# Kernel tuning notes

Hardware: AMD Instinct MI355X
Metric: run time of the kernel (lower is better)

The kernel has to match this reference:

```python
import jax, jax.numpy as jnp
import numpy as np

D_MODEL = 512
N_HEADS = 8
HEAD_DIM = D_MODEL // N_HEADS
SEQ = 2048
BATCH = 2
EPS = 1e-5
SCALE = 1.0 / np.sqrt(HEAD_DIM).astype(np.float32)
# (kind, window, dilation) per head, matching init_kwargs head_specs
SPECS = [("global", 0, 1), ("global", 0, 1),
         ("window", 64, 1), ("window", 128, 1), ("window", 256, 1),
         ("dilated", 64, 2), ("dilated", 64, 4), ("dilated", 64, 8)]


def build_masks(N):
    i = jnp.arange(N)
    D = jnp.abs(i[:, None] - i[None, :])
    ms = []
    for kind, w, dil in SPECS:
        if kind == "global":
            ms.append(jnp.ones((N, N), dtype=bool))
        elif kind == "window":
            ms.append(D <= w)
        else:  # dilated
            ms.append((D % dil == 0) & (D // dil <= w))
    return jnp.stack(ms)  # [H, N, N] bool


def layernorm(x, g, b):
    mu = jnp.mean(x, axis=-1, keepdims=True)
    var = jnp.mean((x - mu) ** 2, axis=-1, keepdims=True)
    return (x - mu) * jax.lax.rsqrt(var + EPS) * g + b


def setup_inputs() -> dict:
    key = jax.random.key(0)
    ks = jax.random.split(key, 7)
    w = 0.02
    return {
        "x": jax.random.normal(ks[0], (BATCH, SEQ, D_MODEL), dtype=jnp.float32),
        "Wq": jax.random.normal(ks[1], (D_MODEL, D_MODEL), dtype=jnp.float32) * w,
        "Wk": jax.random.normal(ks[2], (D_MODEL, D_MODEL), dtype=jnp.float32) * w,
        "Wv": jax.random.normal(ks[3], (D_MODEL, D_MODEL), dtype=jnp.float32) * w,
        "Wo": jax.random.normal(ks[4], (D_MODEL, D_MODEL), dtype=jnp.float32) * w,
        "T_w1": jax.random.normal(ks[5], (D_MODEL, D_MODEL), dtype=jnp.float32) * w,
        "T_b1": jnp.zeros((D_MODEL,), dtype=jnp.float32),
        "T_w2": jax.random.normal(ks[6], (1, D_MODEL), dtype=jnp.float32) * w,
        "T_b2": jnp.zeros((1,), dtype=jnp.float32),
        "ln_in_g": jnp.ones((D_MODEL,), dtype=jnp.float32),
        "ln_in_b": jnp.zeros((D_MODEL,), dtype=jnp.float32),
        "ln_out_g": jnp.ones((D_MODEL,), dtype=jnp.float32),
        "ln_out_b": jnp.zeros((D_MODEL,), dtype=jnp.float32),
    }


def reference(x, Wq, Wk, Wv, Wo, T_w1, T_b1, T_w2, T_b2,
              ln_in_g, ln_in_b, ln_out_g, ln_out_b):
    B, N, H = x.shape
    x0 = x
    xn = layernorm(x, ln_in_g, ln_in_b)
    # torch Linear: y = x @ W.T ; reshape to [B, h, N, d]
    def heads(W):
        return (xn @ W.T).reshape(B, N, N_HEADS, HEAD_DIM).transpose(0, 2, 1, 3)
    Q, K, V = heads(Wq), heads(Wk), heads(Wv)
    attn = jnp.einsum("bhqd,bhkd->bhqk", Q, K) * SCALE
    mask = build_masks(N)  # [h, N, N]
    attn = jnp.where(mask[None], attn, -jnp.inf)
    attn = jax.nn.softmax(attn, axis=-1)  # every row has diagonal unmasked
    out = jnp.einsum("bhqk,bhkd->bhqd", attn, V)
    out = out.transpose(0, 2, 1, 3).reshape(B, N, N_HEADS * HEAD_DIM)
    out = out @ Wo.T
    # tanh-gated softmax over sequence dim
    T_logits = jnp.tanh(xn @ T_w1.T + T_b1) @ T_w2.T + T_b2  # [B, N, 1]
    T = jax.nn.softmax(T_logits, axis=1)
    out = out * T
    return layernorm(out + x0, ln_out_g, ln_out_b)
```

## Files before the change

### kernel.cpp

```cpp
#include <hip/hip_runtime.h>
#include <math.h>

#define N_SEQ 2048
#define DM    512
#define NTOK  4096
#define NH    8
#define HD    64
#define NSLOT 18

typedef __attribute__((ext_vector_type(8))) short short8;
typedef __attribute__((ext_vector_type(4))) short short4_t;
typedef __attribute__((ext_vector_type(4))) float f32x4;

__device__ inline short f2bf(float x) {
    union { float f; unsigned u; } v; v.f = x;
    unsigned r = v.u + 0x7fff + ((v.u >> 16) & 1);
    return (short)(r >> 16);
}
__device__ inline float bf2f(short s) {
    union { unsigned u; float f; } v; v.u = ((unsigned)(unsigned short)s) << 16;
    return v.f;
}
__device__ inline unsigned pkbf(float a, float b) {
    return ((unsigned)(unsigned short)f2bf(b) << 16) | (unsigned)(unsigned short)f2bf(a);
}
__device__ inline float ftanh(float x) {
    float e = __expf(2.f * x);
    return 1.f - 2.f / (e + 1.f);
}

__device__ inline f32x4 mfma16(short8 a, short8 b, f32x4 c) {
    return __builtin_amdgcn_mfma_f32_16x16x32_bf16(a, b, c, 0, 0, 0);
}

__device__ __forceinline__ void async_cp16(const short* g, short* l) {
    __builtin_amdgcn_global_load_lds(
        (const __attribute__((address_space(1))) void*)g,
        (__attribute__((address_space(3))) void*)l, 16, 0, 0);
}

__global__ __launch_bounds__(256) void k_lncvt(
    const float* __restrict__ x, const float* __restrict__ g,
    const float* __restrict__ b, short* __restrict__ y, float* __restrict__ lg,
    const float* __restrict__ Wq, const float* __restrict__ Wk,
    const float* __restrict__ Wv, const float* __restrict__ Tw1,
    const float* __restrict__ Wo,
    short* __restrict__ wcat, short* __restrict__ wo) {
    int blk = blockIdx.x, t = threadIdx.x;
    if (blk < 2048) {
        int sub = t >> 7, tt = t & 127;
        int tk = blk * 2 + sub;
        if (tt == 0) lg[tk] = 0.f;
        float4 xv = ((const float4*)(x + (size_t)tk * DM))[tt];
        float s = xv.x + xv.y + xv.z + xv.w;
        float q = xv.x*xv.x + xv.y*xv.y + xv.z*xv.z + xv.w*xv.w;
        for (int o = 32; o; o >>= 1) { s += __shfl_down(s, o); q += __shfl_down(q, o); }
        __shared__ float ls[4], lq[4];
        if ((t & 63) == 0) { ls[t >> 6] = s; lq[t >> 6] = q; }
        __syncthreads();
        s = ls[sub * 2] + ls[sub * 2 + 1];
        q = lq[sub * 2] + lq[sub * 2 + 1];
        float mu = s * (1.f / DM);
        float var = q * (1.f / DM) - mu * mu;
        float rs = rsqrtf(var + 1e-5f);
        float4 gv = ((const float4*)g)[tt], bv = ((const float4*)b)[tt];
        short4_t o;
        o[0] = f2bf((xv.x - mu) * rs * gv.x + bv.x);
        o[1] = f2bf((xv.y - mu) * rs * gv.y + bv.y);
        o[2] = f2bf((xv.z - mu) * rs * gv.z + bv.z);
        o[3] = f2bf((xv.w - mu) * rs * gv.w + bv.w);
        *(short4_t*)&y[(size_t)tk * DM + tt * 4] = o;
    } else {
        int id = (blk - 2048) * 256 + t;
        if (id < 262144) {
            int z = id >> 16; int off = id & 65535;
            const float* s = (z == 0) ? Wq : (z == 1) ? Wk : (z == 2) ? Wv : Tw1;
            float4 v = ((const float4*)s)[off];
            short4_t o = {f2bf(v.x), f2bf(v.y), f2bf(v.z), f2bf(v.w)};
            *(short4_t*)(wcat + (size_t)z * 262144 + (size_t)off * 4) = o;
        } else {
            int off = id - 262144;
            float4 v = ((const float4*)Wo)[off];
            short4_t o = {f2bf(v.x), f2bf(v.y), f2bf(v.z), f2bf(v.w)};
            *(short4_t*)(wo + (size_t)off * 4) = o;
        }
    }
}

__global__ __launch_bounds__(256) void k_gemmqkvt(
    const short* __restrict__ A, const short* __restrict__ W,
    const float* __restrict__ Tb1, const float* __restrict__ Tw2,
    short* __restrict__ qb, short* __restrict__ kb, short* __restrict__ vb,
    float* __restrict__ lg) {
    __shared__ short As[128 * 32];
    __shared__ short Bs[128 * 32];
    int t = threadIdx.x;
    int lane = t & 63, w = t >> 6;
    int wy = w >> 1, wx = w & 1;
    int ln = lane & 15, q4 = lane >> 4;
    int c0 = blockIdx.x * 128, m0 = blockIdx.y * 128;
    int sr = t >> 2, sc = (t & 3) << 3;
    f32x4 acc[4][4];
    f32x4 zero = {0.f, 0.f, 0.f, 0.f};
    #pragma unroll
    for (int i = 0; i < 4; i++)
        #pragma unroll
        for (int j = 0; j < 4; j++) acc[i][j] = zero;
    for (int k0 = 0; k0 < DM; k0 += 32) {
        __syncthreads();
        async_cp16(&A[(size_t)(m0 + sr) * DM + k0 + sc],      &As[sr * 32 + sc]);
        async_cp16(&A[(size_t)(m0 + 64 + sr) * DM + k0 + sc], &As[(64 + sr) * 32 + sc]);
        async_cp16(&W[(size_t)(c0 + sr) * DM + k0 + sc],      &Bs[sr * 32 + sc]);
        async_cp16(&W[(size_t)(c0 + 64 + sr) * DM + k0 + sc], &Bs[(64 + sr) * 32 + sc]);
        __syncthreads();
        short8 af[4], bfr[4];
        #pragma unroll
        for (int i = 0; i < 4; i++)
            af[i] = *(short8*)&As[(wy * 64 + i * 16 + ln) * 32 + q4 * 8];
        #pragma unroll
        for (int j = 0; j < 4; j++)
            bfr[j] = *(short8*)&Bs[(wx * 64 + j * 16 + ln) * 32 + q4 * 8];
        #pragma unroll
        for (int i = 0; i < 4; i++)
            #pragma unroll
            for (int j = 0; j < 4; j++)
                acc[i][j] = mfma16(af[i], bfr[j], acc[i][j]);
    }
    int z = c0 >> 9;
    if (z < 3) {
        short* dst = (z == 0) ? qb : (z == 1) ? kb : vb;
        float sc2 = (z == 0) ? 0.125f : 1.0f;
        #pragma unroll
        for (int i = 0; i < 4; i++)
            #pragma unroll
            for (int j = 0; j < 4; j++)
                #pragma unroll
                for (int r = 0; r < 4; r++) {
                    int row = m0 + wy * 64 + i * 16 + q4 * 4 + r;
                    int col = c0 + wx * 64 + j * 16 + ln;
                    int nin = col & 511;
                    int h = nin >> 6, d = nin & 63;
                    int bi = row >> 11, n = row & (N_SEQ - 1);
                    dst[(((size_t)bi * NH + h) * N_SEQ + n) * HD + d] =
                        f2bf(acc[i][j][r] * sc2);
                }
    } else {
        #pragma unroll
        for (int i = 0; i < 4; i++) {
            #pragma unroll
            for (int r = 0; r < 4; r++) {
                float s = 0.f;
                #pragma unroll
                for (int j = 0; j < 4; j++) {
                    int tc = (c0 & 511) + wx * 64 + j * 16 + ln;
                    s += ftanh(acc[i][j][r] + Tb1[tc]) * Tw2[tc];
                }
                s += __shfl_xor(s, 1);
                s += __shfl_xor(s, 2);
                s += __shfl_xor(s, 4);
                s += __shfl_xor(s, 8);
                if (ln == 0) {
                    int row = m0 + wy * 64 + i * 16 + q4 * 4 + r;
                    atomicAdd(&lg[row], s);
                }
            }
        }
    }
}

__global__ __launch_bounds__(256) void k_gemmp(
    const short* __restrict__ A, const short* __restrict__ W,
    float* __restrict__ proj) {
    __shared__ short As[128 * 32];
    __shared__ short Bs[64 * 32];
    int t = threadIdx.x;
    int lane = t & 63, w = t >> 6;
    int wy = w >> 1, wx = w & 1;
    int ln = lane & 15, q4 = lane >> 4;
    int c0 = blockIdx.x * 64, m0 = blockIdx.y * 128;
    int sr = t >> 2, sc = (t & 3) << 3;
    int br = t >> 2, bc = (t & 3) << 3;
    f32x4 acc[4][2];
    f32x4 zero = {0.f, 0.f, 0.f, 0.f};
    #pragma unroll
    for (int i = 0; i < 4; i++) { acc[i][0] = zero; acc[i][1] = zero; }
    for (int k0 = 0; k0 < DM; k0 += 32) {
        __syncthreads();
        async_cp16(&A[(size_t)(m0 + sr) * DM + k0 + sc],      &As[sr * 32 + sc]);
        async_cp16(&A[(size_t)(m0 + 64 + sr) * DM + k0 + sc], &As[(64 + sr) * 32 + sc]);
        if (br < 64)
            async_cp16(&W[(size_t)(c0 + br) * DM + k0 + bc], &Bs[br * 32 + bc]);
        __syncthreads();
        short8 af[4], bfr[2];
        #pragma unroll
        for (int i = 0; i < 4; i++)
            af[i] = *(short8*)&As[(wy * 64 + i * 16 + ln) * 32 + q4 * 8];
        #pragma unroll
        for (int j = 0; j < 2; j++)
            bfr[j] = *(short8*)&Bs[(wx * 32 + j * 16 + ln) * 32 + q4 * 8];
        #pragma unroll
        for (int i = 0; i < 4; i++)
            #pragma unroll
            for (int j = 0; j < 2; j++)
                acc[i][j] = mfma16(af[i], bfr[j], acc[i][j]);
    }
    #pragma unroll
    for (int i = 0; i < 4; i++)
        #pragma unroll
        for (int j = 0; j < 2; j++)
            #pragma unroll
            for (int r = 0; r < 4; r++) {
                int row = m0 + wy * 64 + i * 16 + q4 * 4 + r;
                int col = c0 + wx * 32 + j * 16 + ln;
                proj[(size_t)row * DM + col] = acc[i][j][r];
            }
}

__global__ __launch_bounds__(256) void k_vtrgate(const short* __restrict__ vb,
                                                 short* __restrict__ vtb,
                                                 const float* __restrict__ lg,
                                                 float* __restrict__ gate) {
    __shared__ short tile[64][80];
    __shared__ float rg[8];
    int blk = blockIdx.x, t = threadIdx.x;
    if (blk < 512) {
        int n0 = (blk & 31) * 64, bh = blk >> 5;
        const short* src = vb + (size_t)bh * N_SEQ * HD;
        short* dst = vtb + (size_t)bh * HD * N_SEQ;
        #pragma unroll
        for (int i = 0; i < 2; i++) {
            int id = t + 256 * i;
            int r = id >> 3, c = id & 7;
            *(short8*)&tile[r][c * 8] = *(const short8*)&src[(size_t)(n0 + r) * HD + c * 8];
        }
        __syncthreads();
        #pragma unroll
        for (int i = 0; i < 2; i++) {
            int id = t + 256 * i;
            int d = id >> 3, c = id & 7;
            short8 v;
            #pragma unroll
            for (int j = 0; j < 8; j++) v[j] = tile[c * 8 + j][d];
            *(short8*)&dst[(size_t)d * N_SEQ + n0 + c * 8] = v;
        }
    } else {
        int b = blk - 512;
        float v[8];
        {
            float4 a0 = *(const float4*)&lg[b * N_SEQ + t * 8];
            float4 a1 = *(const float4*)&lg[b * N_SEQ + t * 8 + 4];
            v[0] = a0.x; v[1] = a0.y; v[2] = a0.z; v[3] = a0.w;
            v[4] = a1.x; v[5] = a1.y; v[6] = a1.z; v[7] = a1.w;
        }
        float m = v[0];
        #pragma unroll
        for (int j = 1; j < 8; j++) m = fmaxf(m, v[j]);
        for (int o = 32; o; o >>= 1) m = fmaxf(m, __shfl_down(m, o));
        if ((t & 63) == 0) rg[t >> 6] = m;
        __syncthreads();
        m = fmaxf(fmaxf(rg[0], rg[1]), fmaxf(rg[2], rg[3]));
        float e[8], s = 0.f;
        #pragma unroll
        for (int j = 0; j < 8; j++) { e[j] = __expf(v[j] - m); s += e[j]; }
        for (int o = 32; o; o >>= 1) s += __shfl_down(s, o);
        if ((t & 63) == 0) rg[4 + (t >> 6)] = s;
        __syncthreads();
        s = (rg[4] + rg[5]) + (rg[6] + rg[7]);
        float inv = 1.f / s;
        float4 o0 = {e[0] * inv, e[1] * inv, e[2] * inv, e[3] * inv};
        float4 o1 = {e[4] * inv, e[5] * inv, e[6] * inv, e[7] * inv};
        *(float4*)&gate[b * N_SEQ + t * 8] = o0;
        *(float4*)&gate[b * N_SEQ + t * 8 + 4] = o1;
    }
}

__global__ __launch_bounds__(256) void k_attn(const short* __restrict__ qb,
                                              const short* __restrict__ kb,
                                              const short* __restrict__ vtb,
                                              short* __restrict__ P_O,
                                              float* __restrict__ P_ml) {
    __shared__ short Ks[128 * 72];
    __shared__ short Vt[64 * 136];
    __shared__ short Pa[4][16 * 136];
    int t = threadIdx.x;
    int lane = t & 63, w = t >> 6;
    int ln = lane & 15, q4 = lane >> 4;
    int slot = blockIdx.x, qt = blockIdx.y, bi = blockIdx.z;
    int q0 = qt * 64;
    int h, c;
    if (slot < 4)        { h = 0; c = slot; }
    else if (slot < 8)   { h = 1; c = slot - 4; }
    else if (slot == 8)  { h = 2; c = 0; }
    else if (slot == 9)  { h = 3; c = 0; }
    else if (slot < 12)  { h = 4; c = slot - 10; }
    else if (slot == 12) { h = 5; c = 0; }
    else if (slot < 15)  { h = 6; c = slot - 13; }
    else                 { h = 7; c = slot - 15; }
    int kind = (h < 2) ? 0 : (h < 5) ? 1 : 2;
    int wnd = (h == 2 || h >= 5) ? 64 : (h == 3) ? 128 : (h == 4) ? 256 : 0;
    int dsh = (h == 5) ? 1 : (h == 6) ? 2 : (h == 7) ? 3 : 0;
    int dmask = (1 << dsh) - 1;
    int wmax = (kind == 0) ? 0 : (wnd << dsh);
    int tLoU, tHiU, CS;
    if (kind == 0) { tLoU = 0; tHiU = 15; CS = 4; }
    else { tLoU = (q0 - wmax) >> 7; tHiU = (q0 + 63 + wmax) >> 7; CS = 3; }
    int ktLo = tLoU + c * CS;
    int ktHi = ktLo + CS - 1;
    if (ktHi > tHiU) ktHi = tHiU;
    if (ktHi > 15) ktHi = 15;
    if (ktLo < 0) ktLo = 0;
    int p4 = (bi * 32 + qt) * NSLOT + slot;
    float* ml = P_ml + (size_t)p4 * 128;
    if (ktLo > ktHi) {
        if (t < 64) { ml[t] = -1e30f; ml[64 + t] = 0.f; }
        return;
    }
    const size_t base = ((size_t)bi * NH + h) * N_SEQ * HD;
    const short* Q = qb + base;
    const short* K = kb + base;
    const short* Vg = vtb + base;
    short8 qa[2];
    {
        const short* qrow = Q + (size_t)(q0 + w * 16 + ln) * HD + q4 * 8;
        qa[0] = *(const short8*)qrow;
        qa[1] = *(const short8*)(qrow + 32);
    }
    int qi = q0 + w * 16 + ln;
    float m_i = -1e30f, l_i = 0.f;
    f32x4 OT[4];
    f32x4 zero = {0.f, 0.f, 0.f, 0.f};
    #pragma unroll
    for (int d = 0; d < 4; d++) OT[d] = zero;
    short* Paw = Pa[w];
    for (int kt = ktLo; kt <= ktHi; kt++) {
        int k0 = kt << 7;
        __syncthreads();
        #pragma unroll
        for (int i2 = 0; i2 < 4; i2++) {
            int id = t + 256 * i2;
            int kr = id >> 3, cc = id & 7;
            *(short8*)&Ks[kr * 72 + cc * 8] =
                *(const short8*)&K[(size_t)(k0 + kr) * HD + cc * 8];
            int dr = id >> 4, kc = id & 15;
            *(short8*)&Vt[dr * 136 + kc * 8] =
                *(const short8*)&Vg[(size_t)dr * N_SEQ + k0 + kc * 8];
        }
        __syncthreads();
        f32x4 ST[8];
        #pragma unroll
        for (int nt = 0; nt < 8; nt++) ST[nt] = zero;
        #pragma unroll
        for (int nt = 0; nt < 8; nt++) {
            #pragma unroll
            for (int ks = 0; ks < 2; ks++) {
                short8 af = *(short8*)&Ks[(nt * 16 + ln) * 72 + ks * 32 + q4 * 8];
                ST[nt] = mfma16(af, qa[ks], ST[nt]);
            }
        }
        if (kind != 0) {
            #pragma unroll
            for (int nt = 0; nt < 8; nt++)
                #pragma unroll
                for (int r = 0; r < 4; r++) {
                    int key = k0 + nt * 16 + q4 * 4 + r;
                    int dlt = qi - key; dlt = (dlt < 0) ? -dlt : dlt;
                    int valid;
                    if (kind == 1) valid = (dlt <= wnd);
                    else valid = ((dlt & dmask) == 0) && ((dlt >> dsh) <= wnd);
                    if (!valid) ST[nt][r] = -1e30f;
                }
        }
        float rm = -1e30f;
        #pragma unroll
        for (int nt = 0; nt < 8; nt++) {
            float a = fmaxf(ST[nt][0], ST[nt][1]);
            float b = fmaxf(ST[nt][2], ST[nt][3]);
            rm = fmaxf(rm, fmaxf(a, b));
        }
        rm = fmaxf(rm, __shfl_xor(rm, 16));
        rm = fmaxf(rm, __shfl_xor(rm, 32));
        float mn = fmaxf(m_i, rm);
        float sc = __expf(m_i - mn);
        float rs = 0.f;
        #pragma unroll
        for (int nt = 0; nt < 8; nt++) {
            float p0 = __expf(ST[nt][0] - mn);
            float p1 = __expf(ST[nt][1] - mn);
            float p2 = __expf(ST[nt][2] - mn);
            float p3 = __expf(ST[nt][3] - mn);
            rs += (p0 + p1) + (p2 + p3);
            *(unsigned*)&Paw[ln * 136 + nt * 16 + q4 * 4]     = pkbf(p0, p1);
            *(unsigned*)&Paw[ln * 136 + nt * 16 + q4 * 4 + 2] = pkbf(p2, p3);
        }
        rs += __shfl_xor(rs, 16);
        rs += __shfl_xor(rs, 32);
        l_i = l_i * sc + rs;
        m_i = mn;
        #pragma unroll
        for (int d = 0; d < 4; d++) OT[d] *= sc;
        short8 pb[4];
        #pragma unroll
        for (int ks = 0; ks < 4; ks++)
            pb[ks] = *(short8*)&Paw[ln * 136 + ks * 32 + q4 * 8];
        #pragma unroll
        for (int dt = 0; dt < 4; dt++) {
            #pragma unroll
            for (int ks = 0; ks < 4; ks++) {
                short8 a = *(short8*)&Vt[(dt * 16 + ln) * 136 + ks * 32 + q4 * 8];
                OT[dt] = mfma16(a, pb[ks], OT[dt]);
            }
        }
    }
    if (q4 == 0) { ml[w * 16 + ln] = m_i; ml[64 + w * 16 + ln] = l_i; }
    #pragma unroll
    for (int dt = 0; dt < 4; dt++) {
        *(unsigned*)&Paw[ln * 136 + dt * 16 + q4 * 4]     = pkbf(OT[dt][0], OT[dt][1]);
        *(unsigned*)&Paw[ln * 136 + dt * 16 + q4 * 4 + 2] = pkbf(OT[dt][2], OT[dt][3]);
    }
    short8 o0 = *(short8*)&Paw[ln * 136 + q4 * 16];
    short8 o1 = *(short8*)&Paw[ln * 136 + q4 * 16 + 8];
    short* Op = P_O + (size_t)p4 * 4096;
    *(short8*)&Op[(w * 16 + ln) * 64 + q4 * 16] = o0;
    *(short8*)&Op[(w * 16 + ln) * 64 + q4 * 16 + 8] = o1;
}

__global__ __launch_bounds__(256) void k_combine(const short* __restrict__ P_O,
                                                 const float* __restrict__ P_ml,
                                                 short* __restrict__ ob) {
    const int hbase[8] = {0, 4, 8, 9, 10, 12, 13, 15};
    const int hcnt[8]  = {4, 4, 1, 1, 2, 1, 2, 3};
    int h = blockIdx.x, qt = blockIdx.y, bi = blockIdx.z;
    int t = threadIdx.x;
    int row = t >> 2, c0 = (t & 3) * 16;
    int pb = (bi * 32 + qt) * NSLOT + hbase[h];
    int cnt = hcnt[h];
    float m = -1e30f;
    for (int s = 0; s < cnt; s++)
        m = fmaxf(m, P_ml[(size_t)(pb + s) * 128 + row]);
    float l = 0.f;
    float acc[16];
    #pragma unroll
    for (int j = 0; j < 16; j++) acc[j] = 0.f;
    for (int s = 0; s < cnt; s++) {
        float ms = P_ml[(size_t)(pb + s) * 128 + row];
        float ls = P_ml[(size_t)(pb + s) * 128 + 64 + row];
        if (ls > 0.f) {
            float sc = __expf(ms - m);
            l += ls * sc;
            const short* Op = P_O + (size_t)(pb + s) * 4096 + row * 64 + c0;
            short8 v0 = *(const short8*)Op;
            short8 v1 = *(const short8*)(Op + 8);
            #pragma unroll
            for (int j = 0; j < 8; j++) acc[j]     += bf2f(v0[j]) * sc;
            #pragma unroll
            for (int j = 0; j < 8; j++) acc[8 + j] += bf2f(v1[j]) * sc;
        }
    }
    float inv = 1.f / l;
    int n = qt * 64 + row;
    short8 o0, o1;
    #pragma unroll
    for (int j = 0; j < 8; j++) o0[j] = f2bf(acc[j] * inv);
    #pragma unroll
    for (int j = 0; j < 8; j++) o1[j] = f2bf(acc[8 + j] * inv);
    short* dst = ob + ((size_t)bi * N_SEQ + n) * DM + h * 64 + c0;
    *(short8*)dst = o0;
    *(short8*)(dst + 8) = o1;
}

__global__ __launch_bounds__(128) void k_final(const float* __restrict__ proj,
                                               const float* __restrict__ gate,
                                               const float* __restrict__ x0,
                                               const float* __restrict__ g,
                                               const float* __restrict__ b,
                                               float* __restrict__ out) {
    int tk = blockIdx.x, t = threadIdx.x;
    float gt = gate[tk];
    float4 pv = ((const float4*)(proj + (size_t)tk * DM))[t];
    float4 xv = ((const float4*)(x0 + (size_t)tk * DM))[t];
    float4 y;
    y.x = pv.x * gt + xv.x;
    y.y = pv.y * gt + xv.y;
    y.z = pv.z * gt + xv.z;
    y.w = pv.w * gt + xv.w;
    float s = y.x + y.y + y.z + y.w;
    float q = y.x*y.x + y.y*y.y + y.z*y.z + y.w*y.w;
    for (int o = 32; o; o >>= 1) { s += __shfl_down(s, o); q += __shfl_down(q, o); }
    __shared__ float ls[2], lq[2];
    if ((t & 63) == 0) { ls[t >> 6] = s; lq[t >> 6] = q; }
    __syncthreads();
    s = ls[0] + ls[1]; q = lq[0] + lq[1];
    float mu = s * (1.f / DM);
    float var = q * (1.f / DM) - mu * mu;
    float rs = rsqrtf(var + 1e-5f);
    float4 gv = ((const float4*)g)[t], bv = ((const float4*)b)[t];
    float4 o;
    o.x = (y.x - mu) * rs * gv.x + bv.x;
    o.y = (y.y - mu) * rs * gv.y + bv.y;
    o.z = (y.z - mu) * rs * gv.z + bv.z;
    o.w = (y.w - mu) * rs * gv.w + bv.w;
    ((float4*)(out + (size_t)tk * DM))[t] = o;
}

extern "C" void kernel_launch(void* const* d_in, const int* in_sizes, int n_in,
                              void* d_out, int out_size, void* d_ws, size_t ws_size,
                              hipStream_t stream) {
    (void)in_sizes; (void)n_in; (void)out_size; (void)ws_size;
    const float* x    = (const float*)d_in[0];
    const float* Wq   = (const float*)d_in[1];
    const float* Wk   = (const float*)d_in[2];
    const float* Wv   = (const float*)d_in[3];
    const float* Wo   = (const float*)d_in[4];
    const float* Tw1  = (const float*)d_in[5];
    const float* Tb1  = (const float*)d_in[6];
    const float* Tw2  = (const float*)d_in[7];
    const float* ling = (const float*)d_in[9];
    const float* linb = (const float*)d_in[10];
    const float* logg = (const float*)d_in[11];
    const float* logb = (const float*)d_in[12];
    float* out = (float*)d_out;

    const size_t SZ = (size_t)NTOK * DM;
    const int NPART = 2 * 32 * NSLOT;
    char* p = (char*)d_ws;
    short* xn   = (short*)p; p += SZ * 2;
    short* wcat = (short*)p; p += (size_t)2048 * DM * 2;
    short* wo   = (short*)p; p += (size_t)DM * DM * 2;
    short* qb   = (short*)p; p += SZ * 2;
    short* kb   = (short*)p; p += SZ * 2;
    short* vb   = (short*)p; p += SZ * 2;
    short* vtb  = (short*)p; p += SZ * 2;
    short* obuf = (short*)p; p += SZ * 2;
    float* lg   = (float*)p; p += (size_t)NTOK * 4;
    float* gate = (float*)p; p += (size_t)NTOK * 4;
    float* P_ml = (float*)p; p += (size_t)NPART * 128 * 4;
    float* proj = (float*)p;
    short* P_O  = (short*)p; p += (size_t)NPART * 4096 * 2;

    k_lncvt<<<3328, 256, 0, stream>>>(x, ling, linb, xn, lg,
                                      Wq, Wk, Wv, Tw1, Wo, wcat, wo);
    k_gemmqkvt<<<dim3(16, 32), 256, 0, stream>>>(xn, wcat, Tb1, Tw2,
                                                 qb, kb, vb, lg);
    k_vtrgate<<<514, 256, 0, stream>>>(vb, vtb, lg, gate);
    k_attn<<<dim3(NSLOT, 32, 2), 256, 0, stream>>>(qb, kb, vtb, P_O, P_ml);
    k_combine<<<dim3(8, 32, 2), 256, 0, stream>>>(P_O, P_ml, obuf);
    k_gemmp<<<dim3(8, 32), 256, 0, stream>>>(obuf, wo, proj);
    k_final<<<NTOK, 128, 0, stream>>>(proj, gate, x, logg, logb, out);
}
```

Measured before the change: 161.8 us.

## Write V transposed from QKV GEMM, prefetch K/V in attention, fuse gate into combine

```diff
diff --git a/kernel.cpp b/kernel.cpp
--- a/kernel.cpp
+++ b/kernel.cpp
@@ -90,7 +90,7 @@
 __global__ __launch_bounds__(256) void k_gemmqkvt(
     const short* __restrict__ A, const short* __restrict__ W,
     const float* __restrict__ Tb1, const float* __restrict__ Tw2,
-    short* __restrict__ qb, short* __restrict__ kb, short* __restrict__ vb,
+    short* __restrict__ qb, short* __restrict__ kb, short* __restrict__ vtb,
     float* __restrict__ lg) {
     __shared__ short As[128 * 32];
     __shared__ short Bs[128 * 32];
@@ -127,8 +127,8 @@
                 acc[i][j] = mfma16(af[i], bfr[j], acc[i][j]);
     }
     int z = c0 >> 9;
-    if (z < 3) {
-        short* dst = (z == 0) ? qb : (z == 1) ? kb : vb;
+    if (z < 2) {
+        short* dst = (z == 0) ? qb : kb;
         float sc2 = (z == 0) ? 0.125f : 1.0f;
         #pragma unroll
         for (int i = 0; i < 4; i++)
@@ -144,6 +144,20 @@
                     dst[(((size_t)bi * NH + h) * N_SEQ + n) * HD + d] =
                         f2bf(acc[i][j][r] * sc2);
                 }
+    } else if (z == 2) {
+        #pragma unroll
+        for (int i = 0; i < 4; i++) {
+            int row0 = m0 + wy * 64 + i * 16 + q4 * 4;
+            int bi = row0 >> 11, n0 = row0 & (N_SEQ - 1);
+            #pragma unroll
+            for (int j = 0; j < 4; j++) {
+                int nin = (c0 + wx * 64 + j * 16 + ln) & 511;
+                int h = nin >> 6, d = nin & 63;
+                short4_t o = {f2bf(acc[i][j][0]), f2bf(acc[i][j][1]),
+                              f2bf(acc[i][j][2]), f2bf(acc[i][j][3])};
+                *(short4_t*)&vtb[(((size_t)bi * NH + h) * HD + d) * N_SEQ + n0] = o;
+            }
+        }
     } else {
         #pragma unroll
         for (int i = 0; i < 4; i++) {
@@ -214,64 +228,6 @@
                 int col = c0 + wx * 32 + j * 16 + ln;
                 proj[(size_t)row * DM + col] = acc[i][j][r];
             }
-}
-
-__global__ __launch_bounds__(256) void k_vtrgate(const short* __restrict__ vb,
-                                                 short* __restrict__ vtb,
-                                                 const float* __restrict__ lg,
-                                                 float* __restrict__ gate) {
-    __shared__ short tile[64][80];
-    __shared__ float rg[8];
-    int blk = blockIdx.x, t = threadIdx.x;
-    if (blk < 512) {
-        int n0 = (blk & 31) * 64, bh = blk >> 5;
-        const short* src = vb + (size_t)bh * N_SEQ * HD;
-        short* dst = vtb + (size_t)bh * HD * N_SEQ;
-        #pragma unroll
-        for (int i = 0; i < 2; i++) {
-            int id = t + 256 * i;
-            int r = id >> 3, c = id & 7;
-            *(short8*)&tile[r][c * 8] = *(const short8*)&src[(size_t)(n0 + r) * HD + c * 8];
-        }
-        __syncthreads();
-        #pragma unroll
-        for (int i = 0; i < 2; i++) {
-            int id = t + 256 * i;
-            int d = id >> 3, c = id & 7;
-            short8 v;
-            #pragma unroll
-            for (int j = 0; j < 8; j++) v[j] = tile[c * 8 + j][d];
-            *(short8*)&dst[(size_t)d * N_SEQ + n0 + c * 8] = v;
-        }
-    } else {
-        int b = blk - 512;
-        float v[8];
-        {
-            float4 a0 = *(const float4*)&lg[b * N_SEQ + t * 8];
-            float4 a1 = *(const float4*)&lg[b * N_SEQ + t * 8 + 4];
-            v[0] = a0.x; v[1] = a0.y; v[2] = a0.z; v[3] = a0.w;
-            v[4] = a1.x; v[5] = a1.y; v[6] = a1.z; v[7] = a1.w;
-        }
-        float m = v[0];
-        #pragma unroll
-        for (int j = 1; j < 8; j++) m = fmaxf(m, v[j]);
-        for (int o = 32; o; o >>= 1) m = fmaxf(m, __shfl_down(m, o));
-        if ((t & 63) == 0) rg[t >> 6] = m;
-        __syncthreads();
-        m = fmaxf(fmaxf(rg[0], rg[1]), fmaxf(rg[2], rg[3]));
-        float e[8], s = 0.f;
-        #pragma unroll
-        for (int j = 0; j < 8; j++) { e[j] = __expf(v[j] - m); s += e[j]; }
-        for (int o = 32; o; o >>= 1) s += __shfl_down(s, o);
-        if ((t & 63) == 0) rg[4 + (t >> 6)] = s;
-        __syncthreads();
-        s = (rg[4] + rg[5]) + (rg[6] + rg[7]);
-        float inv = 1.f / s;
-        float4 o0 = {e[0] * inv, e[1] * inv, e[2] * inv, e[3] * inv};
-        float4 o1 = {e[4] * inv, e[5] * inv, e[6] * inv, e[7] * inv};
-        *(float4*)&gate[b * N_SEQ + t * 8] = o0;
-        *(float4*)&gate[b * N_SEQ + t * 8 + 4] = o1;
-    }
 }
 
 __global__ __launch_bounds__(256) void k_attn(const short* __restrict__ qb,
@@ -332,20 +288,43 @@
     #pragma unroll
     for (int d = 0; d < 4; d++) OT[d] = zero;
     short* Paw = Pa[w];
-    for (int kt = ktLo; kt <= ktHi; kt++) {
-        int k0 = kt << 7;
-        __syncthreads();
+    int skr = t >> 1, skc = (t & 1) << 3;
+    (void)skr; (void)skc;
+    short8 kreg[4], vreg[4];
+    {
+        int k0 = ktLo << 7;
         #pragma unroll
         for (int i2 = 0; i2 < 4; i2++) {
             int id = t + 256 * i2;
             int kr = id >> 3, cc = id & 7;
-            *(short8*)&Ks[kr * 72 + cc * 8] =
-                *(const short8*)&K[(size_t)(k0 + kr) * HD + cc * 8];
+            kreg[i2] = *(const short8*)&K[(size_t)(k0 + kr) * HD + cc * 8];
             int dr = id >> 4, kc = id & 15;
-            *(short8*)&Vt[dr * 136 + kc * 8] =
-                *(const short8*)&Vg[(size_t)dr * N_SEQ + k0 + kc * 8];
-        }
-        __syncthreads();
+            vreg[i2] = *(const short8*)&Vg[(size_t)dr * N_SEQ + k0 + kc * 8];
+        }
+    }
+    for (int kt = ktLo; kt <= ktHi; kt++) {
+        int k0 = kt << 7;
+        __syncthreads();
+        #pragma unroll
+        for (int i2 = 0; i2 < 4; i2++) {
+            int id = t + 256 * i2;
+            int kr = id >> 3, cc = id & 7;
+            *(short8*)&Ks[kr * 72 + cc * 8] = kreg[i2];
+            int dr = id >> 4, kc = id & 15;
+            *(short8*)&Vt[dr * 136 + kc * 8] = vreg[i2];
+        }
+        __syncthreads();
+        if (kt < ktHi) {
+            int kn = (kt + 1) << 7;
+            #pragma unroll
+            for (int i2 = 0; i2 < 4; i2++) {
+                int id = t + 256 * i2;
+                int kr = id >> 3, cc = id & 7;
+                kreg[i2] = *(const short8*)&K[(size_t)(kn + kr) * HD + cc * 8];
+                int dr = id >> 4, kc = id & 15;
+                vreg[i2] = *(const short8*)&Vg[(size_t)dr * N_SEQ + kn + kc * 8];
+            }
+        }
         f32x4 ST[8];
         #pragma unroll
         for (int nt = 0; nt < 8; nt++) ST[nt] = zero;
@@ -424,48 +403,81 @@
     *(short8*)&Op[(w * 16 + ln) * 64 + q4 * 16 + 8] = o1;
 }
 
-__global__ __launch_bounds__(256) void k_combine(const short* __restrict__ P_O,
-                                                 const float* __restrict__ P_ml,
-                                                 short* __restrict__ ob) {
-    const int hbase[8] = {0, 4, 8, 9, 10, 12, 13, 15};
-    const int hcnt[8]  = {4, 4, 1, 1, 2, 1, 2, 3};
-    int h = blockIdx.x, qt = blockIdx.y, bi = blockIdx.z;
-    int t = threadIdx.x;
-    int row = t >> 2, c0 = (t & 3) * 16;
-    int pb = (bi * 32 + qt) * NSLOT + hbase[h];
-    int cnt = hcnt[h];
-    float m = -1e30f;
-    for (int s = 0; s < cnt; s++)
-        m = fmaxf(m, P_ml[(size_t)(pb + s) * 128 + row]);
-    float l = 0.f;
-    float acc[16];
-    #pragma unroll
-    for (int j = 0; j < 16; j++) acc[j] = 0.f;
-    for (int s = 0; s < cnt; s++) {
-        float ms = P_ml[(size_t)(pb + s) * 128 + row];
-        float ls = P_ml[(size_t)(pb + s) * 128 + 64 + row];
-        if (ls > 0.f) {
-            float sc = __expf(ms - m);
-            l += ls * sc;
-            const short* Op = P_O + (size_t)(pb + s) * 4096 + row * 64 + c0;
-            short8 v0 = *(const short8*)Op;
-            short8 v1 = *(const short8*)(Op + 8);
-            #pragma unroll
-            for (int j = 0; j < 8; j++) acc[j]     += bf2f(v0[j]) * sc;
-            #pragma unroll
-            for (int j = 0; j < 8; j++) acc[8 + j] += bf2f(v1[j]) * sc;
-        }
-    }
-    float inv = 1.f / l;
-    int n = qt * 64 + row;
-    short8 o0, o1;
-    #pragma unroll
-    for (int j = 0; j < 8; j++) o0[j] = f2bf(acc[j] * inv);
-    #pragma unroll
-    for (int j = 0; j < 8; j++) o1[j] = f2bf(acc[8 + j] * inv);
-    short* dst = ob + ((size_t)bi * N_SEQ + n) * DM + h * 64 + c0;
-    *(short8*)dst = o0;
-    *(short8*)(dst + 8) = o1;
+__global__ __launch_bounds__(256) void k_combgate(const short* __restrict__ P_O,
+                                                  const float* __restrict__ P_ml,
+                                                  short* __restrict__ ob,
+                                                  const float* __restrict__ lg,
+                                                  float* __restrict__ gate) {
+    int blk = blockIdx.x, t = threadIdx.x;
+    if (blk < 512) {
+        const int hbase[8] = {0, 4, 8, 9, 10, 12, 13, 15};
+        const int hcnt[8]  = {4, 4, 1, 1, 2, 1, 2, 3};
+        int h = blk & 7, qt = (blk >> 3) & 31, bi = blk >> 8;
+        int row = t >> 2, c0 = (t & 3) * 16;
+        int pb = (bi * 32 + qt) * NSLOT + hbase[h];
+        int cnt = hcnt[h];
+        float m = -1e30f;
+        for (int s = 0; s < cnt; s++)
+            m = fmaxf(m, P_ml[(size_t)(pb + s) * 128 + row]);
+        float l = 0.f;
+        float acc[16];
+        #pragma unroll
+        for (int j = 0; j < 16; j++) acc[j] = 0.f;
+        for (int s = 0; s < cnt; s++) {
+            float ms = P_ml[(size_t)(pb + s) * 128 + row];
+            float ls = P_ml[(size_t)(pb + s) * 128 + 64 + row];
+            if (ls > 0.f) {
+                float sc = __expf(ms - m);
+                l += ls * sc;
+                const short* Op = P_O + (size_t)(pb + s) * 4096 + row * 64 + c0;
+                short8 v0 = *(const short8*)Op;
+                short8 v1 = *(const short8*)(Op + 8);
+                #pragma unroll
+                for (int j = 0; j < 8; j++) acc[j]     += bf2f(v0[j]) * sc;
+                #pragma unroll
+                for (int j = 0; j < 8; j++) acc[8 + j] += bf2f(v1[j]) * sc;
+            }
+        }
+        float inv = 1.f / l;
+        int n = qt * 64 + row;
+        short8 o0, o1;
+        #pragma unroll
+        for (int j = 0; j < 8; j++) o0[j] = f2bf(acc[j] * inv);
+        #pragma unroll
+        for (int j = 0; j < 8; j++) o1[j] = f2bf(acc[8 + j] * inv);
+        short* dst = ob + ((size_t)bi * N_SEQ + n) * DM + h * 64 + c0;
+        *(short8*)dst = o0;
+        *(short8*)(dst + 8) = o1;
+    } else {
+        __shared__ float rg[8];
+        int b = blk - 512;
+        float v[8];
+        {
+            float4 a0 = *(const float4*)&lg[b * N_SEQ + t * 8];
+            float4 a1 = *(const float4*)&lg[b * N_SEQ + t * 8 + 4];
+            v[0] = a0.x; v[1] = a0.y; v[2] = a0.z; v[3] = a0.w;
+            v[4] = a1.x; v[5] = a1.y; v[6] = a1.z; v[7] = a1.w;
+        }
+        float m = v[0];
+        #pragma unroll
+        for (int j = 1; j < 8; j++) m = fmaxf(m, v[j]);
+        for (int o = 32; o; o >>= 1) m = fmaxf(m, __shfl_down(m, o));
+        if ((t & 63) == 0) rg[t >> 6] = m;
+        __syncthreads();
+        m = fmaxf(fmaxf(rg[0], rg[1]), fmaxf(rg[2], rg[3]));
+        float e[8], s = 0.f;
+        #pragma unroll
+        for (int j = 0; j < 8; j++) { e[j] = __expf(v[j] - m); s += e[j]; }
+        for (int o = 32; o; o >>= 1) s += __shfl_down(s, o);
+        if ((t & 63) == 0) rg[4 + (t >> 6)] = s;
+        __syncthreads();
+        s = (rg[4] + rg[5]) + (rg[6] + rg[7]);
+        float inv = 1.f / s;
+        float4 o0 = {e[0] * inv, e[1] * inv, e[2] * inv, e[3] * inv};
+        float4 o1 = {e[4] * inv, e[5] * inv, e[6] * inv, e[7] * inv};
+        *(float4*)&gate[b * N_SEQ + t * 8] = o0;
+        *(float4*)&gate[b * N_SEQ + t * 8 + 4] = o1;
+    }
 }
 
 __global__ __launch_bounds__(128) void k_final(const float* __restrict__ proj,
@@ -528,7 +540,6 @@
     short* wo   = (short*)p; p += (size_t)DM * DM * 2;
     short* qb   = (short*)p; p += SZ * 2;
     short* kb   = (short*)p; p += SZ * 2;
-    short* vb   = (short*)p; p += SZ * 2;
     short* vtb  = (short*)p; p += SZ * 2;
     short* obuf = (short*)p; p += SZ * 2;
     float* lg   = (float*)p; p += (size_t)NTOK * 4;
@@ -540,10 +551,9 @@
     k_lncvt<<<3328, 256, 0, stream>>>(x, ling, linb, xn, lg,
                                       Wq, Wk, Wv, Tw1, Wo, wcat, wo);
     k_gemmqkvt<<<dim3(16, 32), 256, 0, stream>>>(xn, wcat, Tb1, Tw2,
-                                                 qb, kb, vb, lg);
-    k_vtrgate<<<514, 256, 0, stream>>>(vb, vtb, lg, gate);
+                                                 qb, kb, vtb, lg);
     k_attn<<<dim3(NSLOT, 32, 2), 256, 0, stream>>>(qb, kb, vtb, P_O, P_ml);
-    k_combine<<<dim3(8, 32, 2), 256, 0, stream>>>(P_O, P_ml, obuf);
+    k_combgate<<<514, 256, 0, stream>>>(P_O, P_ml, obuf, lg, gate);
     k_gemmp<<<dim3(8, 32), 256, 0, stream>>>(obuf, wo, proj);
     k_final<<<NTOK, 128, 0, stream>>>(proj, gate, x, logg, logb, out);
 }
```

Measured after the change: 162.9 us. Within noise of the previous version (+0.7%).
